# Performance work log

Hardware: AMD Instinct MI355X
Metric: run time of the kernel (lower is better)

## Reference

```python
import jax, jax.numpy as jnp
import numpy as np

SIGMA = 32.0
MAGNITUDE = 1.0


def setup_inputs() -> dict:
    key = jax.random.key(0)
    k1, k2, k3 = jax.random.split(key, 3)
    N = 512
    W = 2048
    L = 2048
    init_vectors = jax.random.normal(k1, (2, N), dtype=jnp.float32)
    x_coord = jax.random.randint(k2, (N,), 0, W)
    y_coord = jax.random.randint(k3, (N,), 0, L)
    return {
        "init_vectors": init_vectors,
        "x_coord": x_coord,
        "y_coord": y_coord,
        "width": W,
        "lenth": L,
    }


def reference(init_vectors, x_coord, y_coord, width, lenth):
    # Scale vectors exactly as the torch module: randn / ((lenth+width)/32) * magnitude
    v = init_vectors * (MAGNITUDE / ((lenth + width) / 32.0))  # [2, N]
    inv2s2 = 1.0 / (2.0 * SIGMA * SIGMA)
    xs = jnp.arange(width, dtype=jnp.float32)   # [W]
    ys = jnp.arange(lenth, dtype=jnp.float32)   # [L]
    xc = x_coord.astype(jnp.float32)            # [N]
    yc = y_coord.astype(jnp.float32)            # [N]
    # Gaussian is separable: exp(-(dx^2+dy^2)/2s^2) = exp(-dx^2/2s^2)*exp(-dy^2/2s^2)
    wx = jnp.exp(-((xs[:, None] - xc[None, :]) ** 2) * inv2s2)  # [W, N]
    wy = jnp.exp(-((ys[:, None] - yc[None, :]) ** 2) * inv2s2)  # [L, N]
    # field[c,x,y] = sum_n wx[x,n] * wy[y,n] * v[c,n]
    t = jnp.einsum("xn,cn->cxn", wx, v)          # [2, W, N] (small)
    field = jnp.einsum("cxn,yn->cxy", t, wy)     # [2, W, L]
    return field[None]                            # [1, 2, W, L]
```

## Files before the change

### kernel.cpp

```cpp
#include <hip/hip_runtime.h>
#include <math.h>


#define N_MAX     512
#define CAND_MAX  192
#define TX        32
#define TY        64
#define HY        32
#define R_CUT     128.0f
#define BATCH     8

#define EXP2F(x) __builtin_amdgcn_exp2f(x)

typedef float f4 __attribute__((ext_vector_type(4)));

__global__ __launch_bounds__(256, 8) void motion_field_kernel(
    const float* __restrict__ init_vectors,
    const int*   __restrict__ x_coord,
    const int*   __restrict__ y_coord,
    const int*   __restrict__ d_width,
    const int*   __restrict__ d_lenth,
    float*       __restrict__ out,
    int N, int W, int L)
{
    __shared__ float s_cx[CAND_MAX], s_cy[CAND_MAX];
    __shared__ float s_cv0[CAND_MAX], s_cv1[CAND_MAX];
    __shared__ int   s_cnt[4];
    __shared__ float s_ex[BATCH][TX];
    __shared__ float s_ey[BATCH][HY];

    const int tid  = threadIdx.x;
    const int wave = tid >> 6;
    const int lane = tid & 63;

    const float scale = 32.0f / (float)(d_width[0] + d_lenth[0]);

    const int x0 = blockIdx.x * TX;
    const int y0 = blockIdx.y * TY;
    const float bx_lo = (float)x0 - R_CUT;
    const float bx_hi = (float)(x0 + TX - 1) + R_CUT;
    const float by_lo = (float)y0 - R_CUT;
    const float by_hi = (float)(y0 + TY - 1) + R_CUT;

    int total = 0;
    for (int base_n = 0; base_n < N; base_n += 256) {
        const int n = base_n + tid;
        bool pred = false;
        float xc = 0.f, yc = 0.f;
        if (n < N) {
            xc = (float)x_coord[n];
            yc = (float)y_coord[n];
            pred = (xc >= bx_lo) && (xc <= bx_hi) && (yc >= by_lo) && (yc <= by_hi);
        }
        const unsigned long long m = __ballot(pred);
        if (lane == 0) s_cnt[wave] = __popcll(m);
        __syncthreads();
        const int c0 = s_cnt[0], c1 = s_cnt[1], c2 = s_cnt[2], c3 = s_cnt[3];
        int base = total;
        if (wave > 0) base += c0;
        if (wave > 1) base += c1;
        if (wave > 2) base += c2;
        if (pred) {
            const int pos = base + __popcll(m & ((1ULL << lane) - 1ULL));
            if (pos < CAND_MAX) {
                s_cx[pos]  = xc;
                s_cy[pos]  = yc;
                s_cv0[pos] = init_vectors[n] * scale;
                s_cv1[pos] = init_vectors[N + n] * scale;
            }
        }
        total += c0 + c1 + c2 + c3;
        __syncthreads();
    }
    const int M = (total < CAND_MAX) ? total : CAND_MAX;

    const int u = tid >> 3;
    const int v = tid & 7;

    const float C2 = -1.4426950408889634f / 2048.0f;
    const size_t WL = (size_t)W * (size_t)L;

    #pragma unroll
    for (int h = 0; h < 2; ++h) {
        const int yh = y0 + h * HY;

        float acc0[4], acc1[4];
        #pragma unroll
        for (int j = 0; j < 4; ++j) { acc0[j] = 0.f; acc1[j] = 0.f; }

        for (int m0 = 0; m0 < M; m0 += BATCH) {
            const int B = (M - m0 < BATCH) ? (M - m0) : BATCH;
            if (tid < B * TX) {
                const int b = tid >> 5, r = tid & (TX - 1);
                const float dx = (float)(x0 + r) - s_cx[m0 + b];
                s_ex[b][r] = EXP2F(dx * dx * C2);
            }
            if (tid < B * HY) {
                const int b = tid >> 5, r = tid & (HY - 1);
                const float dy = (float)(yh + r) - s_cy[m0 + b];
                s_ey[b][r] = EXP2F(dy * dy * C2);
            }
            __syncthreads();

            for (int b = 0; b < B; ++b) {
                const float exu = s_ex[b][u];
                const f4 ey4 = *(const f4*)&s_ey[b][v * 4];
                const float e0 = exu * s_cv0[m0 + b];
                const float e1 = exu * s_cv1[m0 + b];
                const float eys[4] = {ey4.x, ey4.y, ey4.z, ey4.w};
                #pragma unroll
                for (int j = 0; j < 4; ++j) {
                    acc0[j] = fmaf(e0, eys[j], acc0[j]);
                    acc1[j] = fmaf(e1, eys[j], acc1[j]);
                }
            }
            __syncthreads();
        }

        const size_t x  = (size_t)(x0 + u);
        const int yb = yh + v * 4;
        f4 o0 = (f4){acc0[0], acc0[1], acc0[2], acc0[3]};
        f4 o1 = (f4){acc1[0], acc1[1], acc1[2], acc1[3]};
        __builtin_nontemporal_store(o0, (f4*)&out[x * (size_t)L + (size_t)yb]);
        __builtin_nontemporal_store(o1, (f4*)&out[WL + x * (size_t)L + (size_t)yb]);
    }
}

extern "C" void kernel_launch(void* const* d_in, const int* in_sizes, int n_in,
                              void* d_out, int out_size, void* d_ws, size_t ws_size,
                              hipStream_t stream) {
    const float* init_vectors = (const float*)d_in[0];
    const int*   x_coord      = (const int*)d_in[1];
    const int*   y_coord      = (const int*)d_in[2];
    const int*   d_width      = (const int*)d_in[3];
    const int*   d_lenth      = (const int*)d_in[4];
    float*       out          = (float*)d_out;

    const int N = in_sizes[1];
    const int WL = out_size / 2;
    int W = 1;
    while ((long long)W * (long long)W < (long long)WL) W <<= 1;
    const int L = WL / W;

    dim3 grid(W / TX, L / TY);
    dim3 block(256);
    hipLaunchKernelGGL(motion_field_kernel, grid, block, 0, stream,
                       init_vectors, x_coord, y_coord, d_width, d_lenth,
                       out, N, W, L);
}
```

Baseline: 15.21 us.

## Enlarge y-tile and register-block each thread to 2x8 outputs

Each block now covers 32x128 outputs in a single pass over the candidate list, instead of two 32-row halves that each recomputed the exponentials. Each thread accumulates a 2x8 register tile per channel, reusing one shared-memory x-weight and y-weight load across more FMAs. The batch size rises to 16, the candidate cap drops to 96 and the occupancy hint drops to 4 blocks. In exchange, registers per thread rise and the grid has fewer blocks. The lower cap would silently drop Gaussians if a tile ever had more than 96 nearby points.

```diff
diff --git a/kernel.cpp b/kernel.cpp
--- a/kernel.cpp
+++ b/kernel.cpp
@@ -3,18 +3,17 @@
 
 
 #define N_MAX     512
-#define CAND_MAX  192
+#define CAND_MAX  96
 #define TX        32
-#define TY        64
-#define HY        32
+#define TY        128
 #define R_CUT     128.0f
-#define BATCH     8
+#define BATCH     16
 
 #define EXP2F(x) __builtin_amdgcn_exp2f(x)
 
 typedef float f4 __attribute__((ext_vector_type(4)));
 
-__global__ __launch_bounds__(256, 8) void motion_field_kernel(
+__global__ __launch_bounds__(256, 4) void motion_field_kernel(
     const float* __restrict__ init_vectors,
     const int*   __restrict__ x_coord,
     const int*   __restrict__ y_coord,
@@ -27,7 +26,7 @@
     __shared__ float s_cv0[CAND_MAX], s_cv1[CAND_MAX];
     __shared__ int   s_cnt[4];
     __shared__ float s_ex[BATCH][TX];
-    __shared__ float s_ey[BATCH][HY];
+    __shared__ float s_ey[BATCH][TY];
 
     const int tid  = threadIdx.x;
     const int wave = tid >> 6;
@@ -74,55 +73,63 @@
     }
     const int M = (total < CAND_MAX) ? total : CAND_MAX;
 
-    const int u = tid >> 3;
-    const int v = tid & 7;
+    const int u = tid >> 4;
+    const int v = tid & 15;
+
+    f4 acc[2][2][2];
+    #pragma unroll
+    for (int c = 0; c < 2; ++c)
+        #pragma unroll
+        for (int xi = 0; xi < 2; ++xi)
+            #pragma unroll
+            for (int q = 0; q < 2; ++q) acc[c][xi][q] = (f4){0.f,0.f,0.f,0.f};
 
     const float C2 = -1.4426950408889634f / 2048.0f;
+
+    for (int m0 = 0; m0 < M; m0 += BATCH) {
+        const int B = (M - m0 < BATCH) ? (M - m0) : BATCH;
+        for (int s = tid; s < B * TX; s += 256) {
+            const int b = s >> 5, r = s & (TX - 1);
+            const float dx = (float)(x0 + r) - s_cx[m0 + b];
+            s_ex[b][r] = EXP2F(dx * dx * C2);
+        }
+        for (int s = tid; s < B * TY; s += 256) {
+            const int b = s >> 7, r = s & (TY - 1);
+            const float dy = (float)(y0 + r) - s_cy[m0 + b];
+            s_ey[b][r] = EXP2F(dy * dy * C2);
+        }
+        __syncthreads();
+
+        for (int b = 0; b < B; ++b) {
+            const float2 ex2 = *(const float2*)&s_ex[b][u * 2];
+            const f4 eyA = *(const f4*)&s_ey[b][v * 8];
+            const f4 eyB = *(const f4*)&s_ey[b][v * 8 + 4];
+            const float v0 = s_cv0[m0 + b], v1 = s_cv1[m0 + b];
+            const float exs[2] = {ex2.x, ex2.y};
+            #pragma unroll
+            for (int xi = 0; xi < 2; ++xi) {
+                const float e0 = exs[xi] * v0;
+                const float e1 = exs[xi] * v1;
+                acc[0][xi][0] += eyA * e0;
+                acc[0][xi][1] += eyB * e0;
+                acc[1][xi][0] += eyA * e1;
+                acc[1][xi][1] += eyB * e1;
+            }
+        }
+        __syncthreads();
+    }
+
     const size_t WL = (size_t)W * (size_t)L;
-
+    const int yb = y0 + v * 8;
     #pragma unroll
-    for (int h = 0; h < 2; ++h) {
-        const int yh = y0 + h * HY;
-
-        float acc0[4], acc1[4];
+    for (int c = 0; c < 2; ++c) {
         #pragma unroll
-        for (int j = 0; j < 4; ++j) { acc0[j] = 0.f; acc1[j] = 0.f; }
-
-        for (int m0 = 0; m0 < M; m0 += BATCH) {
-            const int B = (M - m0 < BATCH) ? (M - m0) : BATCH;
-            if (tid < B * TX) {
-                const int b = tid >> 5, r = tid & (TX - 1);
-                const float dx = (float)(x0 + r) - s_cx[m0 + b];
-                s_ex[b][r] = EXP2F(dx * dx * C2);
-            }
-            if (tid < B * HY) {
-                const int b = tid >> 5, r = tid & (HY - 1);
-                const float dy = (float)(yh + r) - s_cy[m0 + b];
-                s_ey[b][r] = EXP2F(dy * dy * C2);
-            }
-            __syncthreads();
-
-            for (int b = 0; b < B; ++b) {
-                const float exu = s_ex[b][u];
-                const f4 ey4 = *(const f4*)&s_ey[b][v * 4];
-                const float e0 = exu * s_cv0[m0 + b];
-                const float e1 = exu * s_cv1[m0 + b];
-                const float eys[4] = {ey4.x, ey4.y, ey4.z, ey4.w};
-                #pragma unroll
-                for (int j = 0; j < 4; ++j) {
-                    acc0[j] = fmaf(e0, eys[j], acc0[j]);
-                    acc1[j] = fmaf(e1, eys[j], acc1[j]);
-                }
-            }
-            __syncthreads();
+        for (int xi = 0; xi < 2; ++xi) {
+            const size_t x = (size_t)(x0 + u * 2 + xi);
+            f4* p = (f4*)&out[(size_t)c * WL + x * (size_t)L + (size_t)yb];
+            __builtin_nontemporal_store(acc[c][xi][0], p);
+            __builtin_nontemporal_store(acc[c][xi][1], p + 1);
         }
-
-        const size_t x  = (size_t)(x0 + u);
-        const int yb = yh + v * 4;
-        f4 o0 = (f4){acc0[0], acc0[1], acc0[2], acc0[3]};
-        f4 o1 = (f4){acc1[0], acc1[1], acc1[2], acc1[3]};
-        __builtin_nontemporal_store(o0, (f4*)&out[x * (size_t)L + (size_t)yb]);
-        __builtin_nontemporal_store(o1, (f4*)&out[WL + x * (size_t)L + (size_t)yb]);
     }
 }
 
```

Result: slower. 17.33 us (+13.9%).
